# Kernel tuning notes

Measured on AMD Instinct MI355X. Metric: run time of the kernel, lower is better.

The kernel has to match this reference:

```python
import jax, jax.numpy as jnp
import numpy as np

ALPHA = 0.25
GAMMA = 2.0
EPS = 1e-7


def setup_inputs() -> dict:
    key = jax.random.key(0)
    k1, k2, k3, k4, k5 = jax.random.split(key, 5)
    B, G, A, C = 16, 32, 200000, 1
    # GT boxes: (cx, cy, w, h) in unit image coords, labels all 0 (single face class)
    cxcy = jax.random.uniform(k1, (B, G, 2))
    wh = jax.random.uniform(k2, (B, G, 2)) * 0.3 + 0.01
    labels = jnp.zeros((B, G, 1), dtype=jnp.float32)
    y_true = jnp.concatenate([cxcy, wh, labels], axis=-1)  # [B, G, 5]
    # classifier outputs are probabilities in (0, 1)
    y_classifs = jax.random.uniform(k3, (B, A, C), minval=1e-4, maxval=1.0 - 1e-4)
    y_regressions = jax.random.normal(k4, (B, A, 4))
    # anchors in valid xyxy form
    a1 = jax.random.uniform(k5, (A, 2)) * 0.9
    awh = jax.random.uniform(jax.random.fold_in(k5, 1), (A, 2)) * 0.1 + 0.01
    anchors = jnp.concatenate([a1, a1 + awh], axis=-1)  # [A, 4]
    return {"y_true": y_true, "y_classifs": y_classifs,
            "y_regressions": y_regressions, "anchors": anchors}


def _pairwise_iou(anchors, gt):
    # anchors [A,4] xyxy, gt [G,4] xyxy -> iou [A,G]
    lt = jnp.maximum(anchors[:, None, :2], gt[None, :, :2])
    rb = jnp.minimum(anchors[:, None, 2:], gt[None, :, 2:])
    whi = jnp.clip(rb - lt, 0.0)
    inter = whi[..., 0] * whi[..., 1]
    area_a = (anchors[:, 2] - anchors[:, 0]) * (anchors[:, 3] - anchors[:, 1])
    area_g = (gt[:, 2] - gt[:, 0]) * (gt[:, 3] - gt[:, 1])
    return inter / (area_a[:, None] + area_g[None, :] - inter + 1e-8)


def _per_image_loss(gt5, probs, anchors, num_classes):
    box = gt5[:, :4]                               # [G,4] cxcywh
    label = gt5[:, 4].astype(jnp.int32)            # [G]
    # cxcywh -> xyxy (RetinaNetBoxIoU)
    gt = jnp.concatenate([box[:, :2] - 0.5 * box[:, 2:], box[:, :2] + 0.5 * box[:, 2:]], axis=-1)
    iou = _pairwise_iou(anchors, gt)               # [A,G]
    iou_max = jnp.max(iou, axis=1)                 # [A]
    iou_argmax = jnp.argmax(iou, axis=1)           # [A]
    assigned = label[iou_argmax]                   # [A] class of best-matching GT
    A = probs.shape[0]
    targets = jnp.full((A, num_classes), -1.0, dtype=probs.dtype)
    targets = jnp.where(iou_max[:, None] < 0.4, 0.0, targets)
    pos = iou_max >= 0.5                           # [A]
    pos_onehot = jax.nn.one_hot(assigned, num_classes, dtype=probs.dtype)
    targets = jnp.where(pos[:, None], pos_onehot, targets)
    p = jnp.clip(probs, EPS, 1.0 - EPS)
    alpha_factor = jnp.where(targets == 1.0, ALPHA, 1.0 - ALPHA)
    focal_weight = alpha_factor * jnp.where(targets == 1.0, 1.0 - p, p) ** GAMMA
    bce = -(targets * jnp.log(p) + (1.0 - targets) * jnp.log(1.0 - p))
    cls_loss = jnp.where(targets != -1.0, focal_weight * bce, 0.0)
    num_pos = jnp.maximum(jnp.sum(pos).astype(p.dtype), 1.0)
    return jnp.sum(cls_loss) / num_pos


def reference(y_true, y_classifs, y_regressions, anchors):
    num_classes = y_classifs.shape[-1]
    per_img = jax.vmap(lambda g, p: _per_image_loss(g, p, anchors, num_classes))
    losses = per_img(y_true, y_classifs)           # [B]
    return jnp.mean(losses)
```

## Files before the change

### kernel.cpp

```cpp
#include <hip/hip_runtime.h>
#include <hip/hip_bf16.h>


#define A_N 200000
#define B_N 16
#define G_N 32
#define APT 8
#define BLK 256
#define TILE (BLK * APT)
#define NBX ((A_N + TILE - 1) / TILE)

#define C_POS (0.25f * 0.69314718f)
#define C_NEG (0.75f * 0.69314718f)

__launch_bounds__(BLK)
__global__ void rnl_main(const float4* __restrict__ anchors,
                         const float* __restrict__ probs,
                         const float* __restrict__ y_true,
                         float* __restrict__ ws) {
    __shared__ float4 sbox[G_N];
    __shared__ float  snga[G_N];
    __shared__ float  sga[G_N];
    __shared__ float  slab[G_N];
    __shared__ float  sraw[G_N * 5];
    __shared__ int    sflag;

    const int b = blockIdx.y;
    const int t = threadIdx.x;

    if (t < G_N * 5) sraw[t] = y_true[b * (G_N * 5) + t];
    __syncthreads();
    if (t < 64) {
        float lb = 0.0f;
        if (t < G_N) {
            float cx = sraw[t * 5 + 0], cy = sraw[t * 5 + 1];
            float w  = sraw[t * 5 + 2], h  = sraw[t * 5 + 3];
            lb = sraw[t * 5 + 4];
            float x1 = cx - 0.5f * w, y1 = cy - 0.5f * h;
            float x2 = cx + 0.5f * w, y2 = cy + 0.5f * h;
            float ga = (x2 - x1) * (y2 - y1);
            sbox[t] = make_float4(x1, y1, x2, y2);
            snga[t] = -ga; sga[t] = ga; slab[t] = lb;
        }
        unsigned long long bal = __ballot(lb != 0.0f);
        if (t == 0) sflag = (bal == 0ULL) ? 1 : 0;
    }
    __syncthreads();

    const int base = blockIdx.x * TILE + t;
    const float lab0 = slab[0];

    float loss = 0.0f, cnt = 0.0f;

    float ax[APT], ay[APT], az[APT], aw[APT];
    #pragma unroll
    for (int k = 0; k < APT; ++k) {
        int idx  = base + k * BLK;
        int idxc = idx < A_N ? idx : A_N - 1;
        float4 an = anchors[idxc];
        ax[k] = an.x; ay[k] = an.y; az[k] = an.z; aw[k] = an.w;
    }

    if (sflag) {
        float m1[APT], m2[APT];
        #pragma unroll
        for (int k = 0; k < APT; ++k) { m1[k] = -1e30f; m2[k] = -1e30f; }

        #pragma unroll
        for (int j = 0; j < G_N; ++j) {
            float4 gb  = sbox[j];
            float  nga = snga[j];
            #pragma unroll
            for (int k = 0; k < APT; ++k) {
                float ltx = fmaxf(ax[k], gb.x);
                float lty = fmaxf(ay[k], gb.y);
                float rbx = fminf(az[k], gb.z);
                float rby = fminf(aw[k], gb.w);
                float iw  = fmaxf(rbx - ltx, 0.0f);
                float ih  = fmaxf(rby - lty, 0.0f);
                float inter = iw * ih;
                m1[k] = fmaxf(m1[k], fmaf(inter, 3.0f, nga));
                m2[k] = fmaxf(m2[k], fmaf(inter, 3.5f, nga));
            }
        }
        #pragma unroll
        for (int k = 0; k < APT; ++k) {
            int idx  = base + k * BLK;
            bool valid = idx < A_N;
            int idxc = valid ? idx : A_N - 1;
            float sa = (az[k] - ax[k]) * (aw[k] - ay[k]) + 1e-8f;
            bool pos = m1[k] >= sa;
            bool neg = m2[k] <  sa;
            float p = __builtin_amdgcn_fmed3f(probs[b * A_N + idxc], 1e-7f, 1.0f - 1e-7f);
            float q = 1.0f - p;
            float x = pos ? p : q;
            float w = pos ? C_POS * q * q : C_NEG * p * p;
            float l = w * (-__log2f(x));
            l = ((pos | neg) && valid) ? l : 0.0f;
            loss += l;
            cnt  += (pos && valid) ? 1.0f : 0.0f;
        }
    } else {
        float bi[APT], bS[APT], bl[APT];
        #pragma unroll
        for (int k = 0; k < APT; ++k) {
            bi[k] = 0.0f; bS[k] = 1.0f; bl[k] = lab0;
        }

        #pragma unroll
        for (int j = 0; j < G_N; ++j) {
            float4 gb = sbox[j];
            float  ga = sga[j];
            float  lb = slab[j];
            #pragma unroll
            for (int k = 0; k < APT; ++k) {
                float ltx = fmaxf(ax[k], gb.x);
                float lty = fmaxf(ay[k], gb.y);
                float rbx = fminf(az[k], gb.z);
                float rby = fminf(aw[k], gb.w);
                float iw  = fmaxf(rbx - ltx, 0.0f);
                float ih  = fmaxf(rby - lty, 0.0f);
                float inter = iw * ih;
                float sa = (az[k] - ax[k]) * (aw[k] - ay[k]) + 1e-8f;
                float S  = sa + ga;
                bool better = inter * bS[k] > bi[k] * S;
                bi[k] = better ? inter : bi[k];
                bS[k] = better ? S     : bS[k];
                bl[k] = better ? lb    : bl[k];
            }
        }
        #pragma unroll
        for (int k = 0; k < APT; ++k) {
            int idx  = base + k * BLK;
            bool valid = idx < A_N;
            int idxc = valid ? idx : A_N - 1;
            bool pos = 3.0f * bi[k] >= bS[k];
            bool neg = 3.5f * bi[k] <  bS[k];
            bool tp  = pos && (bl[k] == 0.0f);
            float p = __builtin_amdgcn_fmed3f(probs[b * A_N + idxc], 1e-7f, 1.0f - 1e-7f);
            float q = 1.0f - p;
            float x = tp ? p : q;
            float w = tp ? C_POS * q * q : C_NEG * p * p;
            float l = w * (-__log2f(x));
            l = ((pos | neg) && valid) ? l : 0.0f;
            loss += l;
            cnt  += (pos && valid) ? 1.0f : 0.0f;
        }
    }

    #pragma unroll
    for (int off = 32; off > 0; off >>= 1) {
        loss += __shfl_down(loss, off);
        cnt  += __shfl_down(cnt, off);
    }
    __shared__ float s_l[4], s_c[4];
    int wid  = t >> 6;
    int lane = t & 63;
    if (lane == 0) { s_l[wid] = loss; s_c[wid] = cnt; }
    __syncthreads();
    if (t == 0) {
        atomicAdd(&ws[b],       s_l[0] + s_l[1] + s_l[2] + s_l[3]);
        atomicAdd(&ws[B_N + b], s_c[0] + s_c[1] + s_c[2] + s_c[3]);
    }
}

__global__ void rnl_final(const float* __restrict__ ws, float* __restrict__ out) {
    if (threadIdx.x == 0) {
        float s = 0.0f;
        #pragma unroll
        for (int b = 0; b < B_N; ++b) {
            s += ws[b] / fmaxf(ws[B_N + b], 1.0f);
        }
        out[0] = s * (1.0f / (float)B_N);
    }
}

extern "C" void kernel_launch(void* const* d_in, const int* in_sizes, int n_in,
                              void* d_out, int out_size, void* d_ws, size_t ws_size,
                              hipStream_t stream) {
    const float* y_true     = (const float*)d_in[0];
    const float* y_classifs = (const float*)d_in[1];
    const float* anchors    = (const float*)d_in[3];
    float* ws = (float*)d_ws;

    hipMemsetAsync(ws, 0, 2 * B_N * sizeof(float), stream);

    dim3 grid(NBX, B_N);
    rnl_main<<<grid, BLK, 0, stream>>>((const float4*)anchors, y_classifs,
                                       y_true, ws);

    rnl_final<<<1, 64, 0, stream>>>(ws, (float*)d_out);
}
```

Baseline: 44.43 us.

## Precompute GT box table in prep kernel and hoist prob loads before IoU loop

Adds a small prep kernel that zeroes the accumulators, converts every image's GT boxes to xyxy with areas and labels, and writes a per-image all-zero-label flag into workspace. This replaces the memset call. The main kernel drops its shared-memory setup and both __syncthreads, reading GT values straight from global memory (uniform, likely scalar loads). It also issues the probability loads alongside the anchor loads before the IoU loop so their latency overlaps the compute. The costs are an extra kernel launch and more registers per thread for the prefetched probabilities.

Result: slower. 84.48 us (+90.1%).

```diff
diff --git a/kernel.cpp b/kernel.cpp
--- a/kernel.cpp
+++ b/kernel.cpp
@@ -13,69 +13,74 @@
 #define C_POS (0.25f * 0.69314718f)
 #define C_NEG (0.75f * 0.69314718f)
 
+__global__ void rnl_prep(const float* __restrict__ y_true, float* __restrict__ ws) {
+    const int t = threadIdx.x;
+    if (t < 2 * B_N) ws[t] = 0.0f;
+    if (t < B_N * G_N) {
+        float cx = y_true[t * 5 + 0];
+        float cy = y_true[t * 5 + 1];
+        float w  = y_true[t * 5 + 2];
+        float h  = y_true[t * 5 + 3];
+        float lb = y_true[t * 5 + 4];
+        float x1 = cx - 0.5f * w, y1 = cy - 0.5f * h;
+        float x2 = cx + 0.5f * w, y2 = cy + 0.5f * h;
+        float ga = (x2 - x1) * (y2 - y1);
+        float* e = ws + 2 * B_N + t * 8;
+        e[0] = x1; e[1] = y1; e[2] = x2; e[3] = y2;
+        e[4] = -ga; e[5] = ga; e[6] = lb; e[7] = 0.0f;
+    }
+    __syncthreads();
+    if (t < B_N) {
+        bool allz = true;
+        for (int j = 0; j < G_N; ++j)
+            allz = allz && (y_true[(t * G_N + j) * 5 + 4] == 0.0f);
+        ws[2 * B_N + t * (G_N * 8) + 7] = allz ? 1.0f : 0.0f;
+    }
+}
+
 __launch_bounds__(BLK)
 __global__ void rnl_main(const float4* __restrict__ anchors,
                          const float* __restrict__ probs,
-                         const float* __restrict__ y_true,
+                         const float* __restrict__ gtab,
                          float* __restrict__ ws) {
-    __shared__ float4 sbox[G_N];
-    __shared__ float  snga[G_N];
-    __shared__ float  sga[G_N];
-    __shared__ float  slab[G_N];
-    __shared__ float  sraw[G_N * 5];
-    __shared__ int    sflag;
-
     const int b = blockIdx.y;
     const int t = threadIdx.x;
+    const int base = blockIdx.x * TILE + t;
 
-    if (t < G_N * 5) sraw[t] = y_true[b * (G_N * 5) + t];
-    __syncthreads();
-    if (t < 64) {
-        float lb = 0.0f;
-        if (t < G_N) {
-            float cx = sraw[t * 5 + 0], cy = sraw[t * 5 + 1];
-            float w  = sraw[t * 5 + 2], h  = sraw[t * 5 + 3];
-            lb = sraw[t * 5 + 4];
-            float x1 = cx - 0.5f * w, y1 = cy - 0.5f * h;
-            float x2 = cx + 0.5f * w, y2 = cy + 0.5f * h;
-            float ga = (x2 - x1) * (y2 - y1);
-            sbox[t] = make_float4(x1, y1, x2, y2);
-            snga[t] = -ga; sga[t] = ga; slab[t] = lb;
-        }
-        unsigned long long bal = __ballot(lb != 0.0f);
-        if (t == 0) sflag = (bal == 0ULL) ? 1 : 0;
-    }
-    __syncthreads();
+    const float* __restrict__ g = gtab + b * (G_N * 8);
+    const bool fast = (g[7] != 0.0f);
+    const float lab0 = g[6];
 
-    const int base = blockIdx.x * TILE + t;
-    const float lab0 = slab[0];
-
-    float loss = 0.0f, cnt = 0.0f;
-
-    float ax[APT], ay[APT], az[APT], aw[APT];
+    float ax[APT], ay[APT], az[APT], aw[APT], pv[APT];
     #pragma unroll
     for (int k = 0; k < APT; ++k) {
         int idx  = base + k * BLK;
         int idxc = idx < A_N ? idx : A_N - 1;
         float4 an = anchors[idxc];
         ax[k] = an.x; ay[k] = an.y; az[k] = an.z; aw[k] = an.w;
+        pv[k] = probs[b * A_N + idxc];
     }
 
-    if (sflag) {
+    float loss = 0.0f, cnt = 0.0f;
+
+    if (fast) {
         float m1[APT], m2[APT];
         #pragma unroll
         for (int k = 0; k < APT; ++k) { m1[k] = -1e30f; m2[k] = -1e30f; }
 
         #pragma unroll
         for (int j = 0; j < G_N; ++j) {
-            float4 gb  = sbox[j];
-            float  nga = snga[j];
+            const float gx1 = g[j * 8 + 0];
+            const float gy1 = g[j * 8 + 1];
+            const float gx2 = g[j * 8 + 2];
+            const float gy2 = g[j * 8 + 3];
+            const float nga = g[j * 8 + 4];
             #pragma unroll
             for (int k = 0; k < APT; ++k) {
-                float ltx = fmaxf(ax[k], gb.x);
-                float lty = fmaxf(ay[k], gb.y);
-                float rbx = fminf(az[k], gb.z);
-                float rby = fminf(aw[k], gb.w);
+                float ltx = fmaxf(ax[k], gx1);
+                float lty = fmaxf(ay[k], gy1);
+                float rbx = fminf(az[k], gx2);
+                float rby = fminf(aw[k], gy2);
                 float iw  = fmaxf(rbx - ltx, 0.0f);
                 float ih  = fmaxf(rby - lty, 0.0f);
                 float inter = iw * ih;
@@ -85,13 +90,11 @@
         }
         #pragma unroll
         for (int k = 0; k < APT; ++k) {
-            int idx  = base + k * BLK;
-            bool valid = idx < A_N;
-            int idxc = valid ? idx : A_N - 1;
+            bool valid = (base + k * BLK) < A_N;
             float sa = (az[k] - ax[k]) * (aw[k] - ay[k]) + 1e-8f;
             bool pos = m1[k] >= sa;
             bool neg = m2[k] <  sa;
-            float p = __builtin_amdgcn_fmed3f(probs[b * A_N + idxc], 1e-7f, 1.0f - 1e-7f);
+            float p = __builtin_amdgcn_fmed3f(pv[k], 1e-7f, 1.0f - 1e-7f);
             float q = 1.0f - p;
             float x = pos ? p : q;
             float w = pos ? C_POS * q * q : C_NEG * p * p;
@@ -103,21 +106,22 @@
     } else {
         float bi[APT], bS[APT], bl[APT];
         #pragma unroll
-        for (int k = 0; k < APT; ++k) {
-            bi[k] = 0.0f; bS[k] = 1.0f; bl[k] = lab0;
-        }
+        for (int k = 0; k < APT; ++k) { bi[k] = 0.0f; bS[k] = 1.0f; bl[k] = lab0; }
 
         #pragma unroll
         for (int j = 0; j < G_N; ++j) {
-            float4 gb = sbox[j];
-            float  ga = sga[j];
-            float  lb = slab[j];
+            const float gx1 = g[j * 8 + 0];
+            const float gy1 = g[j * 8 + 1];
+            const float gx2 = g[j * 8 + 2];
+            const float gy2 = g[j * 8 + 3];
+            const float ga  = g[j * 8 + 5];
+            const float lb  = g[j * 8 + 6];
             #pragma unroll
             for (int k = 0; k < APT; ++k) {
-                float ltx = fmaxf(ax[k], gb.x);
-                float lty = fmaxf(ay[k], gb.y);
-                float rbx = fminf(az[k], gb.z);
-                float rby = fminf(aw[k], gb.w);
+                float ltx = fmaxf(ax[k], gx1);
+                float lty = fmaxf(ay[k], gy1);
+                float rbx = fminf(az[k], gx2);
+                float rby = fminf(aw[k], gy2);
                 float iw  = fmaxf(rbx - ltx, 0.0f);
                 float ih  = fmaxf(rby - lty, 0.0f);
                 float inter = iw * ih;
@@ -131,13 +135,11 @@
         }
         #pragma unroll
         for (int k = 0; k < APT; ++k) {
-            int idx  = base + k * BLK;
-            bool valid = idx < A_N;
-            int idxc = valid ? idx : A_N - 1;
+            bool valid = (base + k * BLK) < A_N;
             bool pos = 3.0f * bi[k] >= bS[k];
             bool neg = 3.5f * bi[k] <  bS[k];
             bool tp  = pos && (bl[k] == 0.0f);
-            float p = __builtin_amdgcn_fmed3f(probs[b * A_N + idxc], 1e-7f, 1.0f - 1e-7f);
+            float p = __builtin_amdgcn_fmed3f(pv[k], 1e-7f, 1.0f - 1e-7f);
             float q = 1.0f - p;
             float x = tp ? p : q;
             float w = tp ? C_POS * q * q : C_NEG * p * p;
@@ -183,11 +185,11 @@
     const float* anchors    = (const float*)d_in[3];
     float* ws = (float*)d_ws;
 
-    hipMemsetAsync(ws, 0, 2 * B_N * sizeof(float), stream);
+    rnl_prep<<<1, 512, 0, stream>>>(y_true, ws);
 
     dim3 grid(NBX, B_N);
     rnl_main<<<grid, BLK, 0, stream>>>((const float4*)anchors, y_classifs,
-                                       y_true, ws);
+                                       ws + 2 * B_N, ws);
 
     rnl_final<<<1, 64, 0, stream>>>(ws, (float*)d_out);
 }
```

## Replace atomics and memset with per-block partials and hoist probability loads

Applied to the files above, without the earlier changes.

Each block now writes its loss and positive count to its own slot in workspace instead of doing global atomicAdds. A parallel 256-thread reduce kernel then sums the slots per image, which removes the hipMemsetAsync launch and the atomic contention. Probability loads are also moved up next to the anchor loads so their latency overlaps the IoU loop, at the cost of extra registers.

Result: slower. 67.47 us (+51.9%).

```diff
diff --git a/kernel.cpp b/kernel.cpp
--- a/kernel.cpp
+++ b/kernel.cpp
@@ -17,7 +17,7 @@
 __global__ void rnl_main(const float4* __restrict__ anchors,
                          const float* __restrict__ probs,
                          const float* __restrict__ y_true,
-                         float* __restrict__ ws) {
+                         float2* __restrict__ partials) {
     __shared__ float4 sbox[G_N];
     __shared__ float  snga[G_N];
     __shared__ float  sga[G_N];
@@ -52,13 +52,14 @@
 
     float loss = 0.0f, cnt = 0.0f;
 
-    float ax[APT], ay[APT], az[APT], aw[APT];
+    float ax[APT], ay[APT], az[APT], aw[APT], pv[APT];
     #pragma unroll
     for (int k = 0; k < APT; ++k) {
         int idx  = base + k * BLK;
         int idxc = idx < A_N ? idx : A_N - 1;
         float4 an = anchors[idxc];
         ax[k] = an.x; ay[k] = an.y; az[k] = an.z; aw[k] = an.w;
+        pv[k] = probs[b * A_N + idxc];
     }
 
     if (sflag) {
@@ -85,13 +86,11 @@
         }
         #pragma unroll
         for (int k = 0; k < APT; ++k) {
-            int idx  = base + k * BLK;
-            bool valid = idx < A_N;
-            int idxc = valid ? idx : A_N - 1;
+            bool valid = (base + k * BLK) < A_N;
             float sa = (az[k] - ax[k]) * (aw[k] - ay[k]) + 1e-8f;
             bool pos = m1[k] >= sa;
             bool neg = m2[k] <  sa;
-            float p = __builtin_amdgcn_fmed3f(probs[b * A_N + idxc], 1e-7f, 1.0f - 1e-7f);
+            float p = __builtin_amdgcn_fmed3f(pv[k], 1e-7f, 1.0f - 1e-7f);
             float q = 1.0f - p;
             float x = pos ? p : q;
             float w = pos ? C_POS * q * q : C_NEG * p * p;
@@ -103,9 +102,7 @@
     } else {
         float bi[APT], bS[APT], bl[APT];
         #pragma unroll
-        for (int k = 0; k < APT; ++k) {
-            bi[k] = 0.0f; bS[k] = 1.0f; bl[k] = lab0;
-        }
+        for (int k = 0; k < APT; ++k) { bi[k] = 0.0f; bS[k] = 1.0f; bl[k] = lab0; }
 
         #pragma unroll
         for (int j = 0; j < G_N; ++j) {
@@ -131,13 +128,11 @@
         }
         #pragma unroll
         for (int k = 0; k < APT; ++k) {
-            int idx  = base + k * BLK;
-            bool valid = idx < A_N;
-            int idxc = valid ? idx : A_N - 1;
+            bool valid = (base + k * BLK) < A_N;
             bool pos = 3.0f * bi[k] >= bS[k];
             bool neg = 3.5f * bi[k] <  bS[k];
             bool tp  = pos && (bl[k] == 0.0f);
-            float p = __builtin_amdgcn_fmed3f(probs[b * A_N + idxc], 1e-7f, 1.0f - 1e-7f);
+            float p = __builtin_amdgcn_fmed3f(pv[k], 1e-7f, 1.0f - 1e-7f);
             float q = 1.0f - p;
             float x = tp ? p : q;
             float w = tp ? C_POS * q * q : C_NEG * p * p;
@@ -159,18 +154,33 @@
     if (lane == 0) { s_l[wid] = loss; s_c[wid] = cnt; }
     __syncthreads();
     if (t == 0) {
-        atomicAdd(&ws[b],       s_l[0] + s_l[1] + s_l[2] + s_l[3]);
-        atomicAdd(&ws[B_N + b], s_c[0] + s_c[1] + s_c[2] + s_c[3]);
+        float L = s_l[0] + s_l[1] + s_l[2] + s_l[3];
+        float C = s_c[0] + s_c[1] + s_c[2] + s_c[3];
+        partials[b * NBX + blockIdx.x] = make_float2(L, C);
     }
 }
 
-__global__ void rnl_final(const float* __restrict__ ws, float* __restrict__ out) {
-    if (threadIdx.x == 0) {
+__global__ void rnl_reduce(const float2* __restrict__ partials,
+                           float* __restrict__ out) {
+    const int t = threadIdx.x;
+    const int img = t >> 4, lane16 = t & 15;
+    float L = 0.0f, C = 0.0f;
+    for (int i = lane16; i < NBX; i += 16) {
+        float2 p = partials[img * NBX + i];
+        L += p.x; C += p.y;
+    }
+    #pragma unroll
+    for (int m = 8; m > 0; m >>= 1) {
+        L += __shfl_xor(L, m, 16);
+        C += __shfl_xor(C, m, 16);
+    }
+    __shared__ float sl[B_N], sc[B_N];
+    if (lane16 == 0) { sl[img] = L; sc[img] = C; }
+    __syncthreads();
+    if (t == 0) {
         float s = 0.0f;
         #pragma unroll
-        for (int b = 0; b < B_N; ++b) {
-            s += ws[b] / fmaxf(ws[B_N + b], 1.0f);
-        }
+        for (int b = 0; b < B_N; ++b) s += sl[b] / fmaxf(sc[b], 1.0f);
         out[0] = s * (1.0f / (float)B_N);
     }
 }
@@ -181,13 +191,11 @@
     const float* y_true     = (const float*)d_in[0];
     const float* y_classifs = (const float*)d_in[1];
     const float* anchors    = (const float*)d_in[3];
-    float* ws = (float*)d_ws;
-
-    hipMemsetAsync(ws, 0, 2 * B_N * sizeof(float), stream);
+    float2* partials = (float2*)d_ws;
 
     dim3 grid(NBX, B_N);
     rnl_main<<<grid, BLK, 0, stream>>>((const float4*)anchors, y_classifs,
-                                       y_true, ws);
-
-    rnl_final<<<1, 64, 0, stream>>>(ws, (float*)d_out);
+                                       y_true, partials);
+
+    rnl_reduce<<<1, 256, 0, stream>>>(partials, (float*)d_out);
 }
```
